# Performance work log

Measured on AMD Instinct MI355X. Metric: run time of the kernel, lower is better.

## Reference

```python
import jax, jax.numpy as jnp
import numpy as np

N = 100000
E = 800000
D_IN = 128
D_OUT = 128
EPS = 1e-5


def setup_inputs() -> dict:
    key = jax.random.key(0)
    k = jax.random.split(key, 7)
    x = jax.random.normal(k[0], (N, D_IN), dtype=jnp.float32)
    edge_index = jax.random.randint(k[1], (2, E), 0, N, dtype=jnp.int64)
    # kaiming_uniform(a=sqrt(5)) on [out,in] -> bound = 1/sqrt(in_dim)
    bound = 1.0 / np.sqrt(D_IN)
    W_self = jax.random.uniform(k[2], (D_OUT, D_IN), minval=-bound, maxval=bound, dtype=jnp.float32)
    W_neigh = jax.random.uniform(k[3], (D_OUT, D_IN), minval=-bound, maxval=bound, dtype=jnp.float32)
    bias = jnp.zeros((D_OUT,), dtype=jnp.float32)
    gamma = jnp.ones((D_OUT,), dtype=jnp.float32)
    beta = jnp.zeros((D_OUT,), dtype=jnp.float32)
    return {"x": x, "edge_index": edge_index, "W_self": W_self,
            "W_neigh": W_neigh, "bias": bias, "gamma": gamma, "beta": beta}


def reference(x, edge_index, W_self, W_neigh, bias, gamma, beta):
    src, dst = edge_index[0], edge_index[1]
    # mean neighbor aggregation: segment-sum of gathered features / clamped degree
    agg = jax.ops.segment_sum(x[src], dst, num_segments=N)          # [N, D_IN]
    deg = jax.ops.segment_sum(jnp.ones_like(dst, dtype=x.dtype), dst, num_segments=N)
    neigh_mean = agg / jnp.maximum(deg, 1.0)[:, None]
    # dual linear + bias + ReLU
    out = jnp.einsum('nd,od->no', x, W_self) + jnp.einsum('nd,od->no', neigh_mean, W_neigh) + bias
    h = jax.nn.relu(out)
    # LayerNorm over last dim
    mu = jnp.mean(h, axis=-1, keepdims=True)
    var = jnp.var(h, axis=-1, keepdims=True)
    return (h - mu) * jax.lax.rsqrt(var + EPS) * gamma + beta
```

## Files before the change

kernel.cpp:

```cpp
#include <hip/hip_runtime.h>
#include <hip/hip_bf16.h>

#define N_NODES 100000
#define E_EDGES 800000
#define CAP 32
#define LN_EPS 1e-5f
#define WPAD 264

typedef __attribute__((ext_vector_type(4))) float f32x4;
typedef __attribute__((ext_vector_type(8))) short short8;

__device__ __forceinline__ unsigned short f2bf(float f) {
    __hip_bfloat16 h = __float2bfloat16(f);
    return *reinterpret_cast<unsigned short*>(&h);
}
__device__ __forceinline__ float bflo(unsigned int u) { return __uint_as_float(u << 16); }
__device__ __forceinline__ float bfhi(unsigned int u) { return __uint_as_float(u & 0xffff0000u); }

#define NX4 (N_NODES * 32)
#define NW4 4096
__global__ void convert_kernel(const float* __restrict__ x,
                               const float* __restrict__ Ws,
                               const float* __restrict__ Wn,
                               unsigned short* __restrict__ xb,
                               unsigned short* __restrict__ wsb,
                               unsigned short* __restrict__ wnb) {
    int i = blockIdx.x * blockDim.x + threadIdx.x;
    const float4* src; ushort4* dst; int j;
    if (i < NX4) { src = (const float4*)x; dst = (ushort4*)xb; j = i; }
    else if (i < NX4 + NW4) { src = (const float4*)Ws; dst = (ushort4*)wsb; j = i - NX4; }
    else if (i < NX4 + 2 * NW4) { src = (const float4*)Wn; dst = (ushort4*)wnb; j = i - NX4 - NW4; }
    else return;
    float4 v = src[j];
    ushort4 o; o.x = f2bf(v.x); o.y = f2bf(v.y); o.z = f2bf(v.z); o.w = f2bf(v.w);
    dst[j] = o;
}

__global__ void fill_kernel(const int* __restrict__ ei,
                            int* __restrict__ cnt, int* __restrict__ slots) {
    int e = blockIdx.x * blockDim.x + threadIdx.x;
    if (e >= E_EDGES) return;
    int src = ei[e];
    int dst = ei[E_EDGES + e];
    int p = atomicAdd(&cnt[dst], 1);
    if (p < CAP) slots[dst * CAP + p] = src;
}

__global__ void gather_kernel(const unsigned short* __restrict__ xb,
                              const int* __restrict__ cnt,
                              const int* __restrict__ slots,
                              unsigned short* __restrict__ nb) {
    int node = (blockIdx.x * blockDim.x + threadIdx.x) >> 6;
    int lane = threadIdx.x & 63;
    if (node >= N_NODES) return;
    int c = cnt[node];
    int cc = c > CAP ? CAP : c;
    int myslot = (lane < cc) ? slots[node * CAP + lane] : 0;
    float ax = 0.f, ay = 0.f;
    const unsigned int* xu = reinterpret_cast<const unsigned int*>(xb);
    for (int i = 0; i < cc; ++i) {
        int s = __shfl(myslot, i);
        unsigned int u = xu[s * 64 + lane];
        ax += bflo(u); ay += bfhi(u);
    }
    float inv = 1.0f / (float)(c > 1 ? c : 1);
    ax *= inv; ay *= inv;
    unsigned int o = ((unsigned int)f2bf(ay) << 16) | (unsigned int)f2bf(ax);
    reinterpret_cast<unsigned int*>(nb)[node * 64 + lane] = o;
}

__global__ __launch_bounds__(256, 2) void fused_mfma(
    const unsigned short* __restrict__ xb, const unsigned short* __restrict__ nb,
    const unsigned short* __restrict__ wsb, const unsigned short* __restrict__ wnb,
    const float* __restrict__ bias, const float* __restrict__ gamma,
    const float* __restrict__ beta, float* __restrict__ out)
{
    __shared__ unsigned short WT[128][WPAD];
    const int t = threadIdx.x;
    const ushort4* Ws4 = reinterpret_cast<const ushort4*>(wsb);
    const ushort4* Wn4 = reinterpret_cast<const ushort4*>(wnb);
    for (int idx = t; idx < 4096; idx += 256) {
        int n = idx >> 5, k4 = (idx & 31) << 2;
        *reinterpret_cast<ushort4*>(&WT[n][k4]) = Ws4[idx];
        *reinterpret_cast<ushort4*>(&WT[n][128 + k4]) = Wn4[idx];
    }
    __syncthreads();

    const int lane = t & 63, wave = t >> 6;
    const int l16 = lane & 15, quad = lane >> 4;
    float bia[8], gam[8], bet[8];
#pragma unroll
    for (int n = 0; n < 8; ++n) {
        int col = n * 16 + l16;
        bia[n] = bias[col]; gam[n] = gamma[col]; bet[n] = beta[col];
    }

    const int ntiles = (N_NODES + 255) / 256;
    for (int tile = blockIdx.x; tile < ntiles; tile += gridDim.x) {
        const int rowbase = tile * 256 + wave * 64;
        f32x4 acc[4][8];
#pragma unroll
        for (int m = 0; m < 4; ++m)
#pragma unroll
            for (int n = 0; n < 8; ++n) acc[m][n] = (f32x4)0.f;
        int rows[4];
#pragma unroll
        for (int m = 0; m < 4; ++m) {
            int r = rowbase + m * 16 + l16;
            rows[m] = r < N_NODES ? r : N_NODES - 1;
        }
#pragma unroll
        for (int kstep = 0; kstep < 8; ++kstep) {
            const unsigned short* Asrc = (kstep < 4) ? xb : nb;
            const int koff = (kstep & 3) * 32 + quad * 8;
            short8 a[4];
#pragma unroll
            for (int m = 0; m < 4; ++m)
                a[m] = *reinterpret_cast<const short8*>(Asrc + rows[m] * 128 + koff);
#pragma unroll
            for (int n = 0; n < 8; ++n) {
                short8 b = *reinterpret_cast<const short8*>(&WT[n * 16 + l16][kstep * 32 + quad * 8]);
#pragma unroll
                for (int m = 0; m < 4; ++m)
                    acc[m][n] = __builtin_amdgcn_mfma_f32_16x16x32_bf16(a[m], b, acc[m][n], 0, 0, 0);
            }
        }
#pragma unroll
        for (int m = 0; m < 4; ++m) {
#pragma unroll
            for (int r = 0; r < 4; ++r) {
                float h[8], s = 0.f, q = 0.f;
#pragma unroll
                for (int n = 0; n < 8; ++n) {
                    float v = acc[m][n][r] + bia[n];
                    v = fmaxf(v, 0.f);
                    h[n] = v; s += v; q += v * v;
                }
#pragma unroll
                for (int msk = 1; msk <= 8; msk <<= 1) {
                    s += __shfl_xor(s, msk);
                    q += __shfl_xor(q, msk);
                }
                const float mu = s * (1.f / 128.f);
                const float var = q * (1.f / 128.f) - mu * mu;
                const float rs = rsqrtf(var + LN_EPS);
                const int R = rowbase + m * 16 + quad * 4 + r;
                if (R < N_NODES) {
#pragma unroll
                    for (int n = 0; n < 8; ++n)
                        out[R * 128 + n * 16 + l16] = (h[n] - mu) * rs * gam[n] + bet[n];
                }
            }
        }
    }
}

extern "C" void kernel_launch(void* const* d_in, const int* in_sizes, int n_in,
                              void* d_out, int out_size, void* d_ws, size_t ws_size,
                              hipStream_t stream) {
    const float* x      = (const float*)d_in[0];
    const int*   ei     = (const int*)d_in[1];
    const float* Wself  = (const float*)d_in[2];
    const float* Wneigh = (const float*)d_in[3];
    const float* bias   = (const float*)d_in[4];
    const float* gamma  = (const float*)d_in[5];
    const float* beta   = (const float*)d_in[6];
    float* out = (float*)d_out;

    char* ws = (char*)d_ws;
    int* cnt   = (int*)ws;
    int* slots = (int*)(ws + 400000);
    unsigned short* xb  = (unsigned short*)(ws + 13200000);
    unsigned short* nb  = (unsigned short*)(ws + 38800000);
    unsigned short* wsb = (unsigned short*)(ws + 64400000);
    unsigned short* wnb = (unsigned short*)(ws + 64432768);

    hipMemsetAsync(cnt, 0, N_NODES * sizeof(int), stream);
    convert_kernel<<<(NX4 + 2 * NW4 + 255) / 256, 256, 0, stream>>>(x, Wself, Wneigh, xb, wsb, wnb);
    fill_kernel<<<(E_EDGES + 255) / 256, 256, 0, stream>>>(ei, cnt, slots);
    gather_kernel<<<(N_NODES + 3) / 4, 256, 0, stream>>>(xb, cnt, slots, nb);
    const int ntiles = (N_NODES + 255) / 256;
    fused_mfma<<<ntiles, 256, 0, stream>>>(xb, nb, wsb, wnb, bias, gamma, beta, out);
}
```

Measured before the change: 240.3 us.

## Fuse x conversion with edge fill, widen gather loads, convert weights in-kernel

Merges the bf16 conversion of x and the edge-bucketing fill into one launch so the two independent passes share a single kernel and launch overhead. The weight conversion moves into the MFMA kernel's shared-memory staging, which drops a separate write and read of converted weights. The gather kernel now has each quarter-wave load 16-byte chunks of a different neighbor row, processing four neighbors per iteration, then reduces across quarter-waves with shuffles. In exchange, every MFMA block redundantly converts the fp32 weights, and the gather uses more registers and adds a cross-lane reduction.

```diff
diff --git a/kernel.cpp b/kernel.cpp
--- a/kernel.cpp
+++ b/kernel.cpp
@@ -6,6 +6,7 @@
 #define CAP 32
 #define LN_EPS 1e-5f
 #define WPAD 264
+#define NX4 3200000
 
 typedef __attribute__((ext_vector_type(4))) float f32x4;
 typedef __attribute__((ext_vector_type(8))) short short8;
@@ -17,72 +18,88 @@
 __device__ __forceinline__ float bflo(unsigned int u) { return __uint_as_float(u << 16); }
 __device__ __forceinline__ float bfhi(unsigned int u) { return __uint_as_float(u & 0xffff0000u); }
 
-#define NX4 (N_NODES * 32)
-#define NW4 4096
-__global__ void convert_kernel(const float* __restrict__ x,
-                               const float* __restrict__ Ws,
-                               const float* __restrict__ Wn,
-                               unsigned short* __restrict__ xb,
-                               unsigned short* __restrict__ wsb,
-                               unsigned short* __restrict__ wnb) {
+__global__ __launch_bounds__(256) void prep_kernel(
+    const float* __restrict__ x, const int* __restrict__ ei,
+    unsigned short* __restrict__ xb, int* __restrict__ cnt,
+    int* __restrict__ slots)
+{
     int i = blockIdx.x * blockDim.x + threadIdx.x;
-    const float4* src; ushort4* dst; int j;
-    if (i < NX4) { src = (const float4*)x; dst = (ushort4*)xb; j = i; }
-    else if (i < NX4 + NW4) { src = (const float4*)Ws; dst = (ushort4*)wsb; j = i - NX4; }
-    else if (i < NX4 + 2 * NW4) { src = (const float4*)Wn; dst = (ushort4*)wnb; j = i - NX4 - NW4; }
-    else return;
-    float4 v = src[j];
-    ushort4 o; o.x = f2bf(v.x); o.y = f2bf(v.y); o.z = f2bf(v.z); o.w = f2bf(v.w);
-    dst[j] = o;
+    if (i < NX4) {
+        float4 v = reinterpret_cast<const float4*>(x)[i];
+        ushort4 o;
+        o.x = f2bf(v.x); o.y = f2bf(v.y); o.z = f2bf(v.z); o.w = f2bf(v.w);
+        reinterpret_cast<ushort4*>(xb)[i] = o;
+    } else {
+        int e = i - NX4;
+        if (e >= E_EDGES) return;
+        int src = ei[e];
+        int dst = ei[E_EDGES + e];
+        int p = atomicAdd(&cnt[dst], 1);
+        if (p < CAP) slots[dst * CAP + p] = src;
+    }
 }
 
-__global__ void fill_kernel(const int* __restrict__ ei,
-                            int* __restrict__ cnt, int* __restrict__ slots) {
-    int e = blockIdx.x * blockDim.x + threadIdx.x;
-    if (e >= E_EDGES) return;
-    int src = ei[e];
-    int dst = ei[E_EDGES + e];
-    int p = atomicAdd(&cnt[dst], 1);
-    if (p < CAP) slots[dst * CAP + p] = src;
-}
-
-__global__ void gather_kernel(const unsigned short* __restrict__ xb,
-                              const int* __restrict__ cnt,
-                              const int* __restrict__ slots,
-                              unsigned short* __restrict__ nb) {
+__global__ __launch_bounds__(256) void gather_kernel(
+    const unsigned short* __restrict__ xb, const int* __restrict__ cnt,
+    const int* __restrict__ slots, unsigned short* __restrict__ nb)
+{
     int node = (blockIdx.x * blockDim.x + threadIdx.x) >> 6;
     int lane = threadIdx.x & 63;
     if (node >= N_NODES) return;
     int c = cnt[node];
     int cc = c > CAP ? CAP : c;
     int myslot = (lane < cc) ? slots[node * CAP + lane] : 0;
-    float ax = 0.f, ay = 0.f;
-    const unsigned int* xu = reinterpret_cast<const unsigned int*>(xb);
-    for (int i = 0; i < cc; ++i) {
-        int s = __shfl(myslot, i);
-        unsigned int u = xu[s * 64 + lane];
-        ax += bflo(u); ay += bfhi(u);
+    const int subi = lane >> 4, chunk = lane & 15;
+    float acc[8];
+#pragma unroll
+    for (int k = 0; k < 8; ++k) acc[k] = 0.f;
+    const uint4* x4 = reinterpret_cast<const uint4*>(xb);
+    for (int i = 0; i < cc; i += 4) {
+        int idx = i + subi;
+        int s = __shfl(myslot, idx);
+        uint4 v = x4[s * 16 + chunk];
+        if (idx < cc) {
+            acc[0] += bflo(v.x); acc[1] += bfhi(v.x);
+            acc[2] += bflo(v.y); acc[3] += bfhi(v.y);
+            acc[4] += bflo(v.z); acc[5] += bfhi(v.z);
+            acc[6] += bflo(v.w); acc[7] += bfhi(v.w);
+        }
     }
-    float inv = 1.0f / (float)(c > 1 ? c : 1);
-    ax *= inv; ay *= inv;
-    unsigned int o = ((unsigned int)f2bf(ay) << 16) | (unsigned int)f2bf(ax);
-    reinterpret_cast<unsigned int*>(nb)[node * 64 + lane] = o;
+#pragma unroll
+    for (int k = 0; k < 8; ++k) {
+        acc[k] += __shfl_xor(acc[k], 16);
+        acc[k] += __shfl_xor(acc[k], 32);
+    }
+    if (subi == 0) {
+        float inv = 1.0f / (float)(c > 1 ? c : 1);
+        uint4 o;
+        o.x = ((unsigned)f2bf(acc[1] * inv) << 16) | f2bf(acc[0] * inv);
+        o.y = ((unsigned)f2bf(acc[3] * inv) << 16) | f2bf(acc[2] * inv);
+        o.z = ((unsigned)f2bf(acc[5] * inv) << 16) | f2bf(acc[4] * inv);
+        o.w = ((unsigned)f2bf(acc[7] * inv) << 16) | f2bf(acc[6] * inv);
+        reinterpret_cast<uint4*>(nb)[node * 16 + chunk] = o;
+    }
 }
 
 __global__ __launch_bounds__(256, 2) void fused_mfma(
     const unsigned short* __restrict__ xb, const unsigned short* __restrict__ nb,
-    const unsigned short* __restrict__ wsb, const unsigned short* __restrict__ wnb,
+    const float* __restrict__ Wself, const float* __restrict__ Wneigh,
     const float* __restrict__ bias, const float* __restrict__ gamma,
     const float* __restrict__ beta, float* __restrict__ out)
 {
     __shared__ unsigned short WT[128][WPAD];
     const int t = threadIdx.x;
-    const ushort4* Ws4 = reinterpret_cast<const ushort4*>(wsb);
-    const ushort4* Wn4 = reinterpret_cast<const ushort4*>(wnb);
+    const float4* Ws4 = reinterpret_cast<const float4*>(Wself);
+    const float4* Wn4 = reinterpret_cast<const float4*>(Wneigh);
     for (int idx = t; idx < 4096; idx += 256) {
         int n = idx >> 5, k4 = (idx & 31) << 2;
-        *reinterpret_cast<ushort4*>(&WT[n][k4]) = Ws4[idx];
-        *reinterpret_cast<ushort4*>(&WT[n][128 + k4]) = Wn4[idx];
+        float4 a = Ws4[idx];
+        float4 b = Wn4[idx];
+        ushort4 ua, ub;
+        ua.x = f2bf(a.x); ua.y = f2bf(a.y); ua.z = f2bf(a.z); ua.w = f2bf(a.w);
+        ub.x = f2bf(b.x); ub.y = f2bf(b.y); ub.z = f2bf(b.z); ub.w = f2bf(b.w);
+        *reinterpret_cast<ushort4*>(&WT[n][k4]) = ua;
+        *reinterpret_cast<ushort4*>(&WT[n][128 + k4]) = ub;
     }
     __syncthreads();
 
@@ -172,13 +189,10 @@
     int* slots = (int*)(ws + 400000);
     unsigned short* xb  = (unsigned short*)(ws + 13200000);
     unsigned short* nb  = (unsigned short*)(ws + 38800000);
-    unsigned short* wsb = (unsigned short*)(ws + 64400000);
-    unsigned short* wnb = (unsigned short*)(ws + 64432768);
 
     hipMemsetAsync(cnt, 0, N_NODES * sizeof(int), stream);
-    convert_kernel<<<(NX4 + 2 * NW4 + 255) / 256, 256, 0, stream>>>(x, Wself, Wneigh, xb, wsb, wnb);
-    fill_kernel<<<(E_EDGES + 255) / 256, 256, 0, stream>>>(ei, cnt, slots);
+    prep_kernel<<<(NX4 + E_EDGES + 255) / 256, 256, 0, stream>>>(x, ei, xb, cnt, slots);
     gather_kernel<<<(N_NODES + 3) / 4, 256, 0, stream>>>(xb, cnt, slots, nb);
     const int ntiles = (N_NODES + 255) / 256;
-    fused_mfma<<<ntiles, 256, 0, stream>>>(xb, nb, wsb, wnb, bias, gamma, beta, out);
+    fused_mfma<<<ntiles, 256, 0, stream>>>(xb, nb, Wself, Wneigh, bias, gamma, beta, out);
 }
```

Measured after the change: 219.0 us. 1.1x faster.
